# Kernel optimization log

Measured on AMD Instinct MI355X. Metric: run time of the kernel, lower is better.

## Reference

```python
import jax, jax.numpy as jnp
import numpy as np

NB = 8          # num_bins
HID = 128       # hidden channels of coupling ResidualNet
TB = 3.0        # tail_bound
MINB = 1e-3     # min bin width / height
MIND = 1e-3     # min derivative
DCONST = float(np.log(np.exp(1.0 - MIND) - 1.0))  # softplus(DCONST)+MIND == 1
LU_EPS = 1e-3


def rqs_inverse(x, uw, uh, ud):
    """Inverse monotonic rational-quadratic spline with linear tails (nflows math).
    x: [B,F]; uw,uh broadcastable to [B,F,NB]; ud broadcastable to [B,F,NB-1]."""
    K = NB
    uw = jnp.broadcast_to(uw, x.shape + (K,))
    uh = jnp.broadcast_to(uh, x.shape + (K,))
    ud = jnp.broadcast_to(ud, x.shape + (K - 1,))
    ud = jnp.pad(ud, [(0, 0)] * x.ndim + [(1, 1)], constant_values=DCONST)  # boundary derivs = 1
    inside = (x >= -TB) & (x <= TB)
    xi = jnp.clip(x, -TB, TB)

    def knots(u):
        v = MINB + (1.0 - MINB * K) * jax.nn.softmax(u, -1)
        c = jnp.concatenate([jnp.zeros(x.shape + (1,), x.dtype), jnp.cumsum(v, -1)], -1)
        c = 2.0 * TB * c - TB
        c = c.at[..., 0].set(-TB).at[..., -1].set(TB)
        return c, c[..., 1:] - c[..., :-1]

    cw, w = knots(uw)   # x-knots / bin widths
    ch, h = knots(uh)   # y-knots / bin heights
    d = MIND + jax.nn.softplus(ud)  # [B,F,K+1] knot derivatives

    # searchsorted on cumheights (inverse direction)
    locs = ch.at[..., -1].add(1e-6)
    idx = jnp.clip(jnp.sum((xi[..., None] >= locs).astype(jnp.int32), -1) - 1, 0, K - 1)[..., None]
    g = lambda a: jnp.take_along_axis(a, idx, -1)[..., 0]
    in_cw, in_w, in_ch, in_h = g(cw), g(w), g(ch), g(h)
    delta = in_h / in_w
    d0 = g(d)
    d1 = jnp.take_along_axis(d, idx + 1, -1)[..., 0]

    t = xi - in_ch
    s = d0 + d1 - 2.0 * delta
    a = t * s + in_h * (delta - d0)
    b = in_h * d0 - t * s
    c = -delta * t
    root = (2.0 * c) / (-b - jnp.sqrt(b * b - 4.0 * a * c))
    out = root * in_w + in_cw
    tm = root * (1.0 - root)
    den = delta + s * tm
    dnum = delta ** 2 * (d1 * root ** 2 + 2.0 * delta * tm + d0 * (1.0 - root) ** 2)
    ld = -(jnp.log(dnum) - 2.0 * jnp.log(den))
    return jnp.where(inside, out, x), jnp.where(inside, ld, 0.0)


def resnet(x, Wi, bi, Wb, bb, Wo, bo):
    # nflows ResidualNet: initial linear, 2 pre-activation residual blocks, final linear
    t = x @ Wi + bi
    for j in range(2):
        r = jax.nn.relu(t) @ Wb[2 * j] + bb[2 * j]
        r = jax.nn.relu(r) @ Wb[2 * j + 1] + bb[2 * j + 1]
        t = t + r
    return t @ Wo + bo


def coupling_inverse(z, Wi, bi, Wb, bb, Wo, bo, uw_u, uh_u, ud_u):
    # alternating mask: even dims = identity split, odd dims = transform split
    ident, trans = z[:, 0::2], z[:, 1::2]
    # unconditional spline on identity features is inverted FIRST, then feeds the net
    ident, ld_u = rqs_inverse(ident, uw_u, uh_u, ud_u)
    B, F = trans.shape
    p = resnet(ident, Wi, bi, Wb, bb, Wo, bo).reshape(B, F, 3 * NB - 1)
    scale = 1.0 / np.sqrt(HID)  # nflows divides widths/heights by sqrt(hidden_features)
    trans, ld_t = rqs_inverse(trans, p[..., :NB] * scale, p[..., NB:2 * NB] * scale, p[..., 2 * NB:])
    out = jnp.stack([ident, trans], -1).reshape(B, -1)
    return out, jnp.sum(ld_u, -1) + jnp.sum(ld_t, -1)


def log_prob(x, loc, log_scale, Wi, bi, Wb, bb, Wo, bo, uw_u, uh_u, ud_u,
             lu_lower, lu_upper, lu_ud, lu_b, perms):
    N, T, D = x.shape
    z = x.reshape(-1, D)
    lq = jnp.zeros((z.shape[0],), x.dtype)
    for i in (2, 1, 0):  # flows = [C0,LU0,C1,LU1,C2,LU2]; invert in reverse order
        # LULinearPermute.inverse: permute, then y = L(Ux) + b, logdet = sum log diag(U)
        zp = z[:, perms[i]]
        diag = jax.nn.softplus(lu_ud[i]) + LU_EPS
        U = jnp.triu(lu_upper[i], 1) + jnp.diag(diag)
        L = jnp.tril(lu_lower[i], -1) + jnp.eye(D, dtype=x.dtype)
        z = (zp @ U.T) @ L.T + lu_b[i]
        lq = lq + jnp.sum(jnp.log(diag))
        z, ld = coupling_inverse(z, Wi[i], bi[i], Wb[i], bb[i], Wo[i], bo[i],
                                 uw_u[i], uh_u[i], ud_u[i])
        lq = lq + ld
    # DiagGaussian base log-prob
    lq = lq - 0.5 * D * jnp.log(2.0 * jnp.pi) \
            - jnp.sum(log_scale + 0.5 * ((z - loc) / jnp.exp(log_scale)) ** 2, -1)
    return lq.reshape(N, T)


def setup_inputs():
    key = jax.random.key(0)
    ks = jax.random.split(key, 16)
    N, T, D, F = 8, 512, 550, 275
    OUT = F * (3 * NB - 1)
    s = 0.1
    return {
        "x": jax.random.normal(ks[0], (N, T, D), jnp.float32),
        "loc": 0.1 * jax.random.normal(ks[1], (D,), jnp.float32),
        "log_scale": jnp.zeros((D,), jnp.float32),
        "Wi": s * jax.random.normal(ks[2], (3, F, HID), jnp.float32),
        "bi": jnp.zeros((3, HID), jnp.float32),
        "Wb": s * jax.random.normal(ks[3], (3, 4, HID, HID), jnp.float32),
        "bb": jnp.zeros((3, 4, HID), jnp.float32),
        "Wo": 0.01 * jax.random.normal(ks[4], (3, HID, OUT), jnp.float32),
        "bo": 0.01 * jax.random.normal(ks[5], (3, OUT), jnp.float32),
        "uw_u": jax.random.uniform(ks[6], (3, F, NB), jnp.float32),
        "uh_u": jax.random.uniform(ks[7], (3, F, NB), jnp.float32),
        "ud_u": jax.random.uniform(ks[8], (3, F, NB - 1), jnp.float32),
        "lu_lower": 0.05 * jax.random.normal(ks[9], (3, D, D), jnp.float32),
        "lu_upper": 0.05 * jax.random.normal(ks[10], (3, D, D), jnp.float32),
        "lu_ud": jnp.full((3, D), DCONST, jnp.float32),
        "lu_b": jnp.zeros((3, D), jnp.float32),
        "perms": jnp.stack([jax.random.permutation(ks[11 + i], D) for i in range(3)]).astype(jnp.int32),
    }


def reference(x, loc, log_scale, Wi, bi, Wb, bb, Wo, bo, uw_u, uh_u, ud_u,
              lu_lower, lu_upper, lu_ud, lu_b, perms):
    # log_prob(x).reshape(N, T); calculate_likelihood would just apply exp/nan->0/clamp on top.
    return log_prob(x, loc, log_scale, Wi, bi, Wb, bb, Wo, bo, uw_u, uh_u, ud_u,
                    lu_lower, lu_upper, lu_ud, lu_b, perms)
```

## Files before the change

### kernel.cpp

```cpp
#include <hip/hip_runtime.h>


#define D_DIM 550
#define D_PAD 576
#define N_PAD_A 640
#define F_DIM 275
#define F_PAD 320
#define FP_HALF 288
#define HID_DIM 128
#define OUT_DIM 6325
#define OUT_PAD 6400
#define FT_PAD 276
#define WO2_ROWS (FT_PAD*32)
#define WO_GX (WO2_ROWS/128)
#define B_ROWS 4096
#define NBINS 8
#define TB_C 3.0f
#define MINB_C 0.001f
#define MIND_C 0.001f
#define DCONST_C 0.53974233f
#define LUEPS_C 0.001f
#define RSQRT_HID 0.08838834764831845f

typedef unsigned short ushort_t;
typedef __attribute__((ext_vector_type(8))) short short8;
typedef __attribute__((ext_vector_type(8))) unsigned short ushort8;
typedef __attribute__((ext_vector_type(4))) unsigned short ushort4v;
typedef __attribute__((ext_vector_type(4))) float f32x4;

__device__ __forceinline__ ushort_t f2bf(float f){
    union{float f; unsigned u;} v; v.f = f;
    unsigned r = v.u + 0x7fffu + ((v.u>>16)&1u);
    return (ushort_t)(r>>16);
}
__device__ __forceinline__ float bf2f(ushort_t h){
    union{unsigned u; float f;} v; v.u = ((unsigned)h)<<16;
    return v.f;
}
__device__ __forceinline__ float softplusf(float x){
    return fmaxf(x, 0.f) + __logf(1.f + __expf(-fabsf(x)));
}

__device__ __forceinline__ void knots_from_u(const float* u, float* c, float* w){
    float m = u[0];
#pragma unroll
    for(int k=1;k<NBINS;k++) m = fmaxf(m, u[k]);
    float e[NBINS]; float s = 0.f;
#pragma unroll
    for(int k=0;k<NBINS;k++){ e[k] = __expf(u[k]-m); s += e[k]; }
    float inv = 1.f/s;
    float cum = 0.f;
    c[0] = -TB_C;
#pragma unroll
    for(int k=0;k<NBINS;k++){
        float v = MINB_C + (1.f - MINB_C*(float)NBINS)*e[k]*inv;
        cum += v;
        c[k+1] = 2.f*TB_C*cum - TB_C;
    }
    c[NBINS] = TB_C;
#pragma unroll
    for(int k=0;k<NBINS;k++) w[k] = c[k+1]-c[k];
}

__device__ __forceinline__ void rqs_inv(float x,
                                        const float* cw, const float* w,
                                        const float* ch, const float* h,
                                        const float* d,
                                        float& out, float& ld){
    bool inside = (x >= -TB_C) && (x <= TB_C);
    float xi = fminf(fmaxf(x, -TB_C), TB_C);
    int idx = 0;
#pragma unroll
    for(int j=1;j<NBINS;j++) idx += (xi >= ch[j]) ? 1 : 0;
    float icw=cw[0], iw=w[0], ich=ch[0], ih=h[0], d0=d[0], d1=d[1];
#pragma unroll
    for(int j=1;j<NBINS;j++){
        if(idx==j){ icw=cw[j]; iw=w[j]; ich=ch[j]; ih=h[j]; d0=d[j]; d1=d[j+1]; }
    }
    float delta = ih/iw;
    float t  = xi - ich;
    float s  = d0 + d1 - 2.f*delta;
    float a  = t*s + ih*(delta - d0);
    float b  = ih*d0 - t*s;
    float c  = -delta*t;
    float disc = b*b - 4.f*a*c;
    float root = 2.f*c / (-b - sqrtf(fmaxf(disc, 0.f)));
    float o  = root*iw + icw;
    float tm = root*(1.f-root);
    float den  = delta + s*tm;
    float dnum = delta*delta*(d1*root*root + 2.f*delta*tm + d0*(1.f-root)*(1.f-root));
    float l = 2.f*__logf(den) - __logf(dnum);
    out = inside ? o : x;
    ld  = inside ? l : 0.f;
}


__global__ void build_knots_kernel(const float* __restrict__ uw_u,
                                   const float* __restrict__ uh_u,
                                   const float* __restrict__ ud_u,
                                   float* __restrict__ knots){
    int g = blockIdx.x*blockDim.x + threadIdx.x;
    if(g >= 3*F_DIM) return;
    float* kb = knots + (size_t)g*43;
    float c[9], w[8];
    knots_from_u(uw_u + (size_t)g*8, c, w);
#pragma unroll
    for(int k=0;k<9;k++) kb[k]=c[k];
#pragma unroll
    for(int k=0;k<8;k++) kb[9+k]=w[k];
    knots_from_u(uh_u + (size_t)g*8, c, w);
#pragma unroll
    for(int k=0;k<9;k++) kb[17+k]=c[k];
#pragma unroll
    for(int k=0;k<8;k++) kb[26+k]=w[k];
    float dend = MIND_C + softplusf(DCONST_C);
    kb[34]=dend; kb[42]=dend;
    const float* ud = ud_u + (size_t)g*7;
#pragma unroll
    for(int k=0;k<7;k++) kb[35+k] = MIND_C + softplusf(ud[k]);
}

__global__ void logdiag_kernel(const float* __restrict__ lu_ud, float* __restrict__ outv){
    int tid = threadIdx.x;
    float s = 0.f;
    for(int k=tid; k<3*D_DIM; k+=256) s += __logf(softplusf(lu_ud[k]) + LUEPS_C);
#pragma unroll
    for(int o=32;o>0;o>>=1) s += __shfl_down(s, o);
    __shared__ float sm[4];
    if((tid&63)==0) sm[tid>>6]=s;
    __syncthreads();
    if(tid==0) outv[0] = sm[0]+sm[1]+sm[2]+sm[3];
}

__global__ void build_LU_bf16(const float* __restrict__ lower,
                              const float* __restrict__ upper,
                              const float* __restrict__ ud,
                              const int* __restrict__ perm,
                              ushort_t* __restrict__ Lmb,
                              ushort_t* __restrict__ UpTb){
    int l = blockIdx.z;
    lower += (size_t)l*D_DIM*D_DIM; upper += (size_t)l*D_DIM*D_DIM;
    ud += (size_t)l*D_DIM; perm += (size_t)l*D_DIM;
    Lmb += (size_t)l*N_PAD_A*D_PAD; UpTb += (size_t)l*N_PAD_A*D_PAD;
    int k = blockIdx.x*blockDim.x + threadIdx.x;
    int j = blockIdx.y;
    if(k >= D_DIM) return;
    float lv = (j>k) ? lower[(size_t)j*D_DIM+k] : (j==k ? 1.f : 0.f);
    Lmb[(size_t)j*D_PAD+k] = f2bf(lv);
    float uv;
    if(j<k)       uv = upper[(size_t)j*D_DIM+k];
    else if(j==k) uv = softplusf(ud[k]) + LUEPS_C;
    else          uv = 0.f;
    UpTb[(size_t)perm[k]*D_PAD + j] = f2bf(uv);
}

__global__ void convert_pad(const float* __restrict__ in, ushort_t* __restrict__ out,
                            int M, int K, int Mpad, int Kpad){
    int idx = blockIdx.x*256 + threadIdx.x;
    if(idx >= Mpad*Kpad) return;
    int r = idx / Kpad, c = idx - r*Kpad;
    float v = (r<M && c<K) ? in[(size_t)r*K+c] : 0.f;
    out[idx] = f2bf(v);
}

template<int REMAP>
__global__ void transpose_convert(const float* __restrict__ in, ushort_t* __restrict__ out,
                                  int K, int N, int Kpad, int Npad, long s_in, long s_out){
    in += (size_t)blockIdx.z*s_in; out += (size_t)blockIdx.z*s_out;
    __shared__ float t[32][33];
    int kb = blockIdx.x*32, nb = blockIdx.y*32;
    int tx = threadIdx.x, ty = threadIdx.y;
#pragma unroll
    for(int i=0;i<32;i+=8){
        int k = kb+ty+i, n = nb+tx;
        t[ty+i][tx] = (k<K && n<N) ? in[(size_t)k*N+n] : 0.f;
    }
    __syncthreads();
#pragma unroll
    for(int i=0;i<32;i+=8){
        int n = nb+ty+i, k = kb+tx;
        if(REMAP){
            if(n < OUT_DIM && k < Kpad){
                int f = n/23, j = n - 23*f;
                out[(size_t)(f*32+j)*Kpad+k] = f2bf(t[tx][ty+i]);
            }
        } else if(n<Npad && k<Kpad){
            out[(size_t)n*Kpad+k] = f2bf(t[tx][ty+i]);
        }
    }
}

__global__ void reorder_bias(const float* __restrict__ bo, float* __restrict__ bo2){
    int idx = blockIdx.x*256 + threadIdx.x;
    if(idx >= 3*OUT_DIM) return;
    int l = idx/OUT_DIM, n = idx%OUT_DIM;
    int f = n/23, j = n - 23*f;
    bo2[(size_t)l*WO2_ROWS + f*32 + j] = bo[idx];
}

template<int OUTBF>
__global__ __launch_bounds__(256)
void gemm_mfma(const ushort_t* __restrict__ A, const ushort_t* __restrict__ Bt,
               const float* __restrict__ bias, void* __restrict__ Cv,
               int M, int N, int Kpad, long sA, long sB, long sC){
    A  += (size_t)blockIdx.z*sA;
    Bt += (size_t)blockIdx.z*sB;
    __shared__ ushort_t As[128][72];
    __shared__ ushort_t Bs[128][72];
    int tid = threadIdx.x;
    int row0 = blockIdx.y*128, col0 = blockIdx.x*128;
    int wave = tid>>6, lane = tid&63;
    int wm = wave&1, wn = wave>>1;
    int lm = lane&15, quad = lane>>4;
    f32x4 acc[4][4] = {};
    for(int k0=0; k0<Kpad; k0+=64){
#pragma unroll
        for(int it=0; it<4; it++){
            int c = tid + it*256;
            int r = c>>3, c8 = (c&7)*8;
            *(ushort8*)&As[r][c8] = *(const ushort8*)(A + (size_t)(row0+r)*Kpad + k0 + c8);
            *(ushort8*)&Bs[r][c8] = *(const ushort8*)(Bt + (size_t)(col0+r)*Kpad + k0 + c8);
        }
        __syncthreads();
#pragma unroll
        for(int ks=0; ks<2; ks++){
            short8 af[4], bfr[4];
#pragma unroll
            for(int i=0;i<4;i++){
                af[i]  = *(const short8*)&As[wm*64 + i*16 + lm][ks*32 + quad*8];
                bfr[i] = *(const short8*)&Bs[wn*64 + i*16 + lm][ks*32 + quad*8];
            }
#pragma unroll
            for(int i=0;i<4;i++)
#pragma unroll
                for(int j=0;j<4;j++)
                    acc[i][j] = __builtin_amdgcn_mfma_f32_16x16x32_bf16(af[i], bfr[j], acc[i][j], 0, 0, 0);
        }
        __syncthreads();
    }
#pragma unroll
    for(int i=0;i<4;i++){
        int rbase = row0 + wm*64 + i*16 + quad*4;
#pragma unroll
        for(int j=0;j<4;j++){
            int gc = col0 + wn*64 + j*16 + lm;
            if(gc >= N) continue;
            float bv = bias[gc];
#pragma unroll
            for(int r=0;r<4;r++){
                int gr = rbase + r;
                float v = acc[i][j][r] + bv;
                if(OUTBF) ((ushort_t*)Cv + (size_t)blockIdx.z*sC)[(size_t)gr*N+gc] = f2bf(v);
                else      ((float*)Cv + (size_t)blockIdx.z*sC)[(size_t)gr*N+gc] = v;
            }
        }
    }
}

__global__ __launch_bounds__(256)
void resnet_fused(const ushort_t* __restrict__ identb,
                  const ushort_t* __restrict__ WiT,
                  const float* __restrict__ bi,
                  const ushort_t* __restrict__ WbT,
                  const float* __restrict__ bb,
                  ushort_t* __restrict__ tb){
    __shared__ __align__(16) char smem[(64*136 + 128*136)*2];
    ushort_t (*As2)[136] = (ushort_t(*)[136])smem;
    ushort_t (*Ws)[136]  = (ushort_t(*)[136])(smem + 64*136*2);
    ushort_t (*As1)[72]  = (ushort_t(*)[72])smem;
    ushort_t (*Bs1)[72]  = (ushort_t(*)[72])(smem + 64*136*2);
    int tid = threadIdx.x, wave = tid>>6, lane = tid&63;
    int lm = lane&15, quad = lane>>4;
    int r0 = blockIdx.x*64;
    f32x4 cur[8] = {};
    f32x4 tsv[8];
    for(int k0=0; k0<F_PAD; k0+=64){
#pragma unroll
        for(int it=0; it<2; it++){
            int v = tid + it*256; int r = v>>3, c8 = (v&7)*8;
            *(ushort8*)&As1[r][c8] = *(const ushort8*)(identb + (size_t)(r0+r)*F_PAD + k0 + c8);
        }
#pragma unroll
        for(int it=0; it<4; it++){
            int v = tid + it*256; int n = v>>3, c8 = (v&7)*8;
            *(ushort8*)&Bs1[n][c8] = *(const ushort8*)(WiT + (size_t)n*F_PAD + k0 + c8);
        }
        __syncthreads();
#pragma unroll
        for(int ks=0; ks<2; ks++){
            short8 af = *(const short8*)&As1[wave*16 + lm][ks*32 + quad*8];
#pragma unroll
            for(int j=0;j<8;j++){
                short8 bf = *(const short8*)&Bs1[j*16 + lm][ks*32 + quad*8];
                cur[j] = __builtin_amdgcn_mfma_f32_16x16x32_bf16(af, bf, cur[j], 0, 0, 0);
            }
        }
        __syncthreads();
    }
#pragma unroll
    for(int j=0;j<8;j++){
        float bv = bi[j*16 + lm];
#pragma unroll
        for(int r=0;r<4;r++) cur[j][r] += bv;
        tsv[j] = cur[j];
    }
    for(int st=0; st<4; st++){
#pragma unroll
        for(int j=0;j<8;j++)
#pragma unroll
            for(int r=0;r<4;r++)
                As2[wave*16 + quad*4 + r][j*16 + lm] = f2bf(fmaxf(cur[j][r], 0.f));
#pragma unroll
        for(int it=0; it<8; it++){
            int v = tid + it*256; int n = v>>4, c8 = (v&15)*8;
            *(ushort8*)&Ws[n][c8] = *(const ushort8*)(WbT + (size_t)st*128*128 + (size_t)n*128 + c8);
        }
        __syncthreads();
        f32x4 acc[8] = {};
#pragma unroll
        for(int ks=0; ks<4; ks++){
            short8 af = *(const short8*)&As2[wave*16 + lm][ks*32 + quad*8];
#pragma unroll
            for(int j=0;j<8;j++){
                short8 bf = *(const short8*)&Ws[j*16 + lm][ks*32 + quad*8];
                acc[j] = __builtin_amdgcn_mfma_f32_16x16x32_bf16(af, bf, acc[j], 0, 0, 0);
            }
        }
        __syncthreads();
#pragma unroll
        for(int j=0;j<8;j++){
            float bv = bb[st*128 + j*16 + lm];
#pragma unroll
            for(int r=0;r<4;r++) acc[j][r] += bv;
        }
        if(st==1 || st==3){
#pragma unroll
            for(int j=0;j<8;j++){
#pragma unroll
                for(int r=0;r<4;r++) acc[j][r] += tsv[j][r];
                tsv[j] = acc[j];
            }
        }
#pragma unroll
        for(int j=0;j<8;j++) cur[j] = acc[j];
    }
#pragma unroll
    for(int j=0;j<8;j++)
#pragma unroll
        for(int r=0;r<4;r++)
            tb[(size_t)(r0 + wave*16 + quad*4 + r)*HID_DIM + j*16 + lm] = f2bf(cur[j][r]);
}

__global__ __launch_bounds__(256)
void zodd_transpose(const float* __restrict__ z2, float* __restrict__ z2oddT){
    __shared__ float s[32][65];
    int r0 = blockIdx.x*64, f0 = blockIdx.y*32;
    int tid = threadIdx.x;
    int f = tid & 31, rb = tid >> 5;
#pragma unroll
    for(int rr=0; rr<8; rr++){
        int r = rb + rr*8;
        int fg = f0 + f;
        float v = (fg < F_DIM) ? z2[(size_t)(r0+r)*D_DIM + 2*fg + 1] : 0.f;
        s[f][r] = v;
    }
    __syncthreads();
    int lane = tid & 63, fb = tid >> 6;
#pragma unroll
    for(int ff=0; ff<8; ff++){
        int fo = fb + ff*4;
        z2oddT[(size_t)(f0+fo)*B_ROWS + r0 + lane] = s[fo][lane];
    }
}

__global__ __launch_bounds__(256, 2)
void wo_spline(const ushort_t* __restrict__ tb,
               const ushort_t* __restrict__ Wo2,
               const float* __restrict__ bo2,
               const float* __restrict__ z2oddT,
               ushort_t* __restrict__ zOddT,
               float* __restrict__ ldpart){
    __shared__ __align__(16) char smem[128*133*4];
    __shared__ float ldred[128];
    ushort_t (*As)[72] = (ushort_t(*)[72])smem;
    ushort_t (*Bs)[72] = (ushort_t(*)[72])(smem + 128*72*2);
    float (*P)[133] = (float(*)[133])smem;
    int tid = threadIdx.x;
    int flat = blockIdx.y*WO_GX + blockIdx.x;
    int flat2 = (flat & 7)*(WO_GX*32/8) + (flat >> 3);
    int cbl = flat2 % WO_GX;
    int rbl = flat2 / WO_GX;
    int row0 = rbl*128, col0 = cbl*128;
    int wave = tid>>6, lane = tid&63;
    int wm = wave&1, wn = wave>>1;
    int lm = lane&15, quad = lane>>4;
    f32x4 acc[4][4] = {};
    for(int k0=0; k0<HID_DIM; k0+=64){
#pragma unroll
        for(int it=0; it<4; it++){
            int c = tid + it*256;
            int r = c>>3, c8 = (c&7)*8;
            *(ushort8*)&As[r][c8] = *(const ushort8*)(tb + (size_t)(row0+r)*HID_DIM + k0 + c8);
            *(ushort8*)&Bs[r][c8] = *(const ushort8*)(Wo2 + (size_t)(col0+r)*HID_DIM + k0 + c8);
        }
        __syncthreads();
#pragma unroll
        for(int ks=0; ks<2; ks++){
            short8 af[4], bfr[4];
#pragma unroll
            for(int i=0;i<4;i++){
                af[i]  = *(const short8*)&As[wm*64 + i*16 + lm][ks*32 + quad*8];
                bfr[i] = *(const short8*)&Bs[wn*64 + i*16 + lm][ks*32 + quad*8];
            }
#pragma unroll
            for(int i=0;i<4;i++)
#pragma unroll
                for(int j=0;j<4;j++)
                    acc[i][j] = __builtin_amdgcn_mfma_f32_16x16x32_bf16(af[i], bfr[j], acc[i][j], 0, 0, 0);
        }
        __syncthreads();
    }
#pragma unroll
    for(int j=0;j<4;j++){
        int cl = wn*64 + j*16 + lm;
        float bv = bo2[col0 + cl];
#pragma unroll
        for(int i=0;i<4;i++){
            int rl = wm*64 + i*16 + quad*4;
#pragma unroll
            for(int r=0;r<4;r++) P[rl+r][cl] = acc[i][j][r] + bv;
        }
    }
    __syncthreads();
    int row = tid & 127;
    int fbase = col0 >> 5;
    float ldsum = 0.f;
    const float dend = MIND_C + softplusf(DCONST_C);
#pragma unroll
    for(int e2=0;e2<2;e2++){
        int feat = (tid>>7) + e2*2;
        int fg = fbase + feat;
        if(fg < F_DIM){
            const float* q = &P[row][feat*32];
            float xv = z2oddT[(size_t)fg*B_ROWS + row0 + row];
            bool inside = (xv >= -TB_C) && (xv <= TB_C);
            float xi = fminf(fmaxf(xv, -TB_C), TB_C);
            float eh[8];
            float mh = -1e30f, sh = 0.f;
#pragma unroll
            for(int k=0;k<8;k++){ float u = q[8+k]*RSQRT_HID; eh[k]=u; mh=fmaxf(mh,u); }
#pragma unroll
            for(int k=0;k<8;k++){ eh[k] = __expf(eh[k]-mh); sh += eh[k]; }
            float invh = (1.f - MINB_C*8.f)/sh;
            int idx = 0;
            {
                float cum = 0.f;
#pragma unroll
                for(int k=0;k<7;k++){
                    cum += MINB_C + eh[k]*invh;
                    float ck = 2.f*TB_C*cum - TB_C;
                    idx += (xi >= ck) ? 1 : 0;
                }
            }
            float ich = -TB_C, ihh = 0.f;
            {
                float cum = 0.f, cprev = -TB_C;
#pragma unroll
                for(int k=0;k<8;k++){
                    cum += MINB_C + eh[k]*invh;
                    float ck = (k==7) ? TB_C : (2.f*TB_C*cum - TB_C);
                    if(idx==k){ ich = cprev; ihh = ck - cprev; }
                    cprev = ck;
                }
            }
            float ew[8];
            float mw = -1e30f, sw = 0.f;
#pragma unroll
            for(int k=0;k<8;k++){ float u = q[k]*RSQRT_HID; ew[k]=u; mw=fmaxf(mw,u); }
#pragma unroll
            for(int k=0;k<8;k++){ ew[k] = __expf(ew[k]-mw); sw += ew[k]; }
            float invw = (1.f - MINB_C*8.f)/sw;
            float icw = -TB_C, iww = 0.f;
            {
                float cum = 0.f, cprev = -TB_C;
#pragma unroll
                for(int k=0;k<8;k++){
                    cum += MINB_C + ew[k]*invw;
                    float ck = (k==7) ? TB_C : (2.f*TB_C*cum - TB_C);
                    if(idx==k){ icw = cprev; iww = ck - cprev; }
                    cprev = ck;
                }
            }
            float d0 = (idx==0) ? dend : (MIND_C + softplusf(q[15+idx]));
            float d1 = (idx==7) ? dend : (MIND_C + softplusf(q[16+idx]));
            float delta = ihh/iww;
            float t  = xi - ich;
            float s  = d0 + d1 - 2.f*delta;
            float a  = t*s + ihh*(delta - d0);
            float b  = ihh*d0 - t*s;
            float c  = -delta*t;
            float disc = fmaxf(b*b - 4.f*a*c, 0.f);
            float root = 2.f*c / (-b - sqrtf(disc));
            float o  = root*iww + icw;
            float tm = root*(1.f-root);
            float den  = delta + s*tm;
            float dnum = delta*delta*(d1*root*root + 2.f*delta*tm + d0*(1.f-root)*(1.f-root));
            float l = 2.f*__logf(den) - __logf(dnum);
            zOddT[(size_t)fg*B_ROWS + row0 + row] = f2bf(inside ? o : xv);
            ldsum += inside ? l : 0.f;
        }
    }
    if(tid >= 128) ldred[tid-128] = ldsum;
    __syncthreads();
    if(tid < 128) ldpart[(size_t)cbl*B_ROWS + row0 + tid] = ldsum + ldred[tid];
}

__global__ __launch_bounds__(256)
void interleave_z(const ushort_t* __restrict__ identb,
                  const ushort_t* __restrict__ zOddT,
                  const float* __restrict__ ldpart,
                  ushort_t* __restrict__ znb,
                  float* __restrict__ lq){
    __shared__ ushort_t s[FP_HALF][34];
    int r0 = blockIdx.x*32;
    int tid = threadIdx.x;
#pragma unroll
    for(int i=0;i<36;i++){
        int idx = tid + i*256;
        int f = idx>>5, r = idx&31;
        s[f][r] = zOddT[(size_t)f*B_ROWS + r0 + r];
    }
    __syncthreads();
    int wv = tid>>6, lane = tid&63;
#pragma unroll
    for(int k=0;k<8;k++){
        int r = wv + k*4;
        const ushort_t* idr = identb + (size_t)(r0+r)*F_PAD;
        unsigned* orow = (unsigned*)(znb + (size_t)(r0+r)*D_PAD);
#pragma unroll
        for(int c=0;c<5;c++){
            int f = lane + c*64;
            if(f < FP_HALF){
                unsigned lo = idr[f];
                unsigned hi = s[f][r];
                orow[f] = lo | (hi<<16);
            }
        }
    }
    if(tid < 32){
        float acc = 0.f;
        for(int cb=0; cb<WO_GX; cb++)
            acc += ldpart[(size_t)cb*B_ROWS + r0 + tid];
        lq[r0 + tid] += acc;
    }
}


__global__ __launch_bounds__(320)
void ident_spline_kernel(const float* __restrict__ z2, const float* __restrict__ knots,
                         int layer, ushort_t* __restrict__ identb,
                         float* __restrict__ lq){
    int row = blockIdx.x; int tid = threadIdx.x;
    float ldv = 0.f;
    if(tid < F_DIM){
        const float* kb = knots + ((size_t)(layer*F_DIM + tid))*43;
        float x = z2[(size_t)row*D_DIM + 2*tid];
        float o, l;
        rqs_inv(x, kb, kb+9, kb+17, kb+26, kb+34, o, l);
        identb[(size_t)row*F_PAD + tid] = f2bf(o);
        ldv = l;
    } else {
        identb[(size_t)row*F_PAD + tid] = 0;
    }
    __shared__ float sm[5];
    float v = ldv;
#pragma unroll
    for(int o=32;o>0;o>>=1) v += __shfl_down(v, o);
    if((tid&63)==0) sm[tid>>6]=v;
    __syncthreads();
    if(tid==0) lq[row] += sm[0]+sm[1]+sm[2]+sm[3]+sm[4];
}

__global__ __launch_bounds__(320)
void finalize_kernel(const ushort_t* __restrict__ zb, const float* __restrict__ loc,
                     const float* __restrict__ lsc, const float* __restrict__ lq,
                     const float* __restrict__ logdiag, float* __restrict__ out){
    int row = blockIdx.x; int tid = threadIdx.x;
    float s = 0.f;
    for(int k=tid; k<D_DIM; k+=320){
        float l = lsc[k];
        float diff = (bf2f(zb[(size_t)row*D_PAD+k])-loc[k])*__expf(-l);
        s += l + 0.5f*diff*diff;
    }
    __shared__ float sm[5];
#pragma unroll
    for(int o=32;o>0;o>>=1) s += __shfl_down(s, o);
    if((tid&63)==0) sm[tid>>6]=s;
    __syncthreads();
    if(tid==0){
        float tot = sm[0]+sm[1]+sm[2]+sm[3]+sm[4];
        out[row] = lq[row] + logdiag[0] - 275.f*1.8378770664f - tot;
    }
}


extern "C" void kernel_launch(void* const* d_in, const int* in_sizes, int n_in,
                              void* d_out, int out_size, void* d_ws, size_t ws_size,
                              hipStream_t stream){
    const float* x        = (const float*)d_in[0];
    const float* loc      = (const float*)d_in[1];
    const float* lsc      = (const float*)d_in[2];
    const float* Wi       = (const float*)d_in[3];
    const float* bi       = (const float*)d_in[4];
    const float* Wb       = (const float*)d_in[5];
    const float* bb       = (const float*)d_in[6];
    const float* Wo       = (const float*)d_in[7];
    const float* bo       = (const float*)d_in[8];
    const float* uw_u     = (const float*)d_in[9];
    const float* uh_u     = (const float*)d_in[10];
    const float* ud_u     = (const float*)d_in[11];
    const float* lu_lower = (const float*)d_in[12];
    const float* lu_upper = (const float*)d_in[13];
    const float* lu_ud    = (const float*)d_in[14];
    const float* lu_b     = (const float*)d_in[15];
    const int*   perms    = (const int*)d_in[16];
    float* out = (float*)d_out;

    char* base = (char*)d_ws;
    size_t off = 0;
    auto alloc = [&](size_t bytes)->char*{
        char* p = base + off;
        off += (bytes + 255) & ~(size_t)255;
        return p;
    };
    float* lq      = (float*)alloc(B_ROWS*4);
    float* zbias   = (float*)alloc(D_PAD*4);
    float* logdiag = (float*)alloc(64*4);
    float* knots   = (float*)alloc((size_t)3*F_DIM*43*4);
    float* z2      = (float*)alloc((size_t)B_ROWS*D_DIM*4);
    float* z2oddT  = (float*)alloc((size_t)FP_HALF*B_ROWS*4);
    float* ldpart  = (float*)alloc((size_t)WO_GX*B_ROWS*4);
    float* bo2     = (float*)alloc((size_t)3*WO2_ROWS*4);
    ushort_t* xb   = (ushort_t*)alloc((size_t)B_ROWS*D_PAD*2);
    ushort_t* zbf0 = (ushort_t*)alloc((size_t)B_ROWS*D_PAD*2);
    ushort_t* zbf1 = (ushort_t*)alloc((size_t)B_ROWS*D_PAD*2);
    ushort_t* zOddT= (ushort_t*)alloc((size_t)FP_HALF*B_ROWS*2);
    ushort_t* Lmb  = (ushort_t*)alloc((size_t)3*N_PAD_A*D_PAD*2);
    ushort_t* UpTb = (ushort_t*)alloc((size_t)3*N_PAD_A*D_PAD*2);
    ushort_t* Apb  = (ushort_t*)alloc((size_t)3*N_PAD_A*D_PAD*2);
    ushort_t* identb=(ushort_t*)alloc((size_t)B_ROWS*F_PAD*2);
    ushort_t* tb   = (ushort_t*)alloc((size_t)B_ROWS*HID_DIM*2);
    ushort_t* WiT  = (ushort_t*)alloc((size_t)3*HID_DIM*F_PAD*2);
    ushort_t* WbT  = (ushort_t*)alloc((size_t)3*4*HID_DIM*HID_DIM*2);
    ushort_t* Wo2  = (ushort_t*)alloc((size_t)3*WO2_ROWS*HID_DIM*2);

    hipMemsetAsync(lq, 0, B_ROWS*sizeof(float), stream);
    hipMemsetAsync(zbias, 0, D_PAD*sizeof(float), stream);
    hipMemsetAsync(zOddT, 0, (size_t)FP_HALF*B_ROWS*2, stream);
    hipMemsetAsync(Lmb, 0, (size_t)3*N_PAD_A*D_PAD*2, stream);
    hipMemsetAsync(UpTb, 0, (size_t)3*N_PAD_A*D_PAD*2, stream);
    hipMemsetAsync(Wo2, 0, (size_t)3*WO2_ROWS*HID_DIM*2, stream);
    hipMemsetAsync(bo2, 0, (size_t)3*WO2_ROWS*4, stream);
    build_knots_kernel<<<dim3((3*F_DIM+255)/256), dim3(256), 0, stream>>>(uw_u, uh_u, ud_u, knots);
    logdiag_kernel<<<dim3(1), dim3(256), 0, stream>>>(lu_ud, logdiag);
    convert_pad<<<dim3((B_ROWS*D_PAD+255)/256), dim3(256), 0, stream>>>(
        x, xb, B_ROWS, D_DIM, B_ROWS, D_PAD);
    build_LU_bf16<<<dim3((D_DIM+255)/256, D_DIM, 3), dim3(256), 0, stream>>>(
        lu_lower, lu_upper, lu_ud, perms, Lmb, UpTb);
    gemm_mfma<1><<<dim3(5, 5, 3), dim3(256), 0, stream>>>(
        Lmb, UpTb, zbias, Apb, N_PAD_A, D_PAD, D_PAD,
        (long)N_PAD_A*D_PAD, (long)N_PAD_A*D_PAD, (long)N_PAD_A*D_PAD);
    dim3 tthr(32,8);
    transpose_convert<0><<<dim3(F_PAD/32, HID_DIM/32, 3), tthr, 0, stream>>>(
        Wi, WiT, F_DIM, HID_DIM, F_PAD, HID_DIM, (long)F_DIM*HID_DIM, (long)F_PAD*HID_DIM);
    transpose_convert<0><<<dim3(HID_DIM/32, HID_DIM/32, 12), tthr, 0, stream>>>(
        Wb, WbT, HID_DIM, HID_DIM, HID_DIM, HID_DIM, (long)HID_DIM*HID_DIM, (long)HID_DIM*HID_DIM);
    transpose_convert<1><<<dim3(HID_DIM/32, OUT_PAD/32, 3), tthr, 0, stream>>>(
        Wo, Wo2, HID_DIM, OUT_DIM, HID_DIM, OUT_PAD, (long)HID_DIM*OUT_DIM, (long)WO2_ROWS*HID_DIM);
    reorder_bias<<<dim3((3*OUT_DIM+255)/256), dim3(256), 0, stream>>>(bo, bo2);

    const ushort_t* zcur_b = xb;
    ushort_t* zbf[2] = {zbf0, zbf1};
    int zi = 0;

    for(int it=0; it<3; ++it){
        int i = 2 - it;

        gemm_mfma<0><<<dim3(N_PAD_A/128, B_ROWS/128), dim3(256), 0, stream>>>(
            zcur_b, Apb + (size_t)i*N_PAD_A*D_PAD, lu_b + (size_t)i*D_DIM,
            z2, B_ROWS, D_DIM, D_PAD, 0, 0, 0);

        zodd_transpose<<<dim3(B_ROWS/64, FP_HALF/32), dim3(256), 0, stream>>>(
            z2, z2oddT);

        ident_spline_kernel<<<dim3(B_ROWS), dim3(320), 0, stream>>>(
            z2, knots, i, identb, lq);

        resnet_fused<<<dim3(B_ROWS/64), dim3(256), 0, stream>>>(
            identb, WiT + (size_t)i*HID_DIM*F_PAD, bi + (size_t)i*HID_DIM,
            WbT + (size_t)i*4*HID_DIM*HID_DIM, bb + (size_t)i*4*HID_DIM, tb);

        wo_spline<<<dim3(WO_GX, B_ROWS/128), dim3(256), 0, stream>>>(
            tb, Wo2 + (size_t)i*WO2_ROWS*HID_DIM, bo2 + (size_t)i*WO2_ROWS,
            z2oddT, zOddT, ldpart);

        interleave_z<<<dim3(B_ROWS/32), dim3(256), 0, stream>>>(
            identb, zOddT, ldpart, zbf[zi], lq);

        zcur_b = zbf[zi];
        zi ^= 1;
    }

    finalize_kernel<<<dim3(B_ROWS), dim3(320), 0, stream>>>(
        zcur_b, loc, lsc, lq, logdiag, out);
}
```

Baseline: 434.5 us.

## Shrink resnet row tile to 16, keep weights in registers, tile-transpose UT build

The fused ResNet kernel now handles 16 rows per block instead of 64, launching four times as many blocks. Each wave owns two output column tiles and loads its weight fragments straight from global memory into registers, double-buffering the next stage's weights, so shared memory holds only the 16-row activation tile. Separately, building the permuted transposed U matrix is split into its own kernel that transposes through a shared-memory tile, which avoids the scattered strided writes of the old combined kernel. The aim is more parallelism and less shared-memory traffic, at the cost of each block re-reading the weights from global memory or L2.

```diff
diff --git a/kernel.cpp b/kernel.cpp
--- a/kernel.cpp
+++ b/kernel.cpp
@@ -132,26 +132,45 @@
     if(tid==0) outv[0] = sm[0]+sm[1]+sm[2]+sm[3];
 }
 
-__global__ void build_LU_bf16(const float* __restrict__ lower,
-                              const float* __restrict__ upper,
-                              const float* __restrict__ ud,
-                              const int* __restrict__ perm,
-                              ushort_t* __restrict__ Lmb,
-                              ushort_t* __restrict__ UpTb){
+__global__ void build_L_bf16(const float* __restrict__ lower,
+                             ushort_t* __restrict__ Lmb){
     int l = blockIdx.z;
-    lower += (size_t)l*D_DIM*D_DIM; upper += (size_t)l*D_DIM*D_DIM;
-    ud += (size_t)l*D_DIM; perm += (size_t)l*D_DIM;
-    Lmb += (size_t)l*N_PAD_A*D_PAD; UpTb += (size_t)l*N_PAD_A*D_PAD;
+    lower += (size_t)l*D_DIM*D_DIM;
+    Lmb += (size_t)l*N_PAD_A*D_PAD;
     int k = blockIdx.x*blockDim.x + threadIdx.x;
     int j = blockIdx.y;
     if(k >= D_DIM) return;
     float lv = (j>k) ? lower[(size_t)j*D_DIM+k] : (j==k ? 1.f : 0.f);
     Lmb[(size_t)j*D_PAD+k] = f2bf(lv);
-    float uv;
-    if(j<k)       uv = upper[(size_t)j*D_DIM+k];
-    else if(j==k) uv = softplusf(ud[k]) + LUEPS_C;
-    else          uv = 0.f;
-    UpTb[(size_t)perm[k]*D_PAD + j] = f2bf(uv);
+}
+
+__global__ void build_UT_bf16(const float* __restrict__ upper,
+                              const float* __restrict__ ud,
+                              const int* __restrict__ perm,
+                              ushort_t* __restrict__ UpTb){
+    int l = blockIdx.z;
+    upper += (size_t)l*D_DIM*D_DIM; ud += (size_t)l*D_DIM; perm += (size_t)l*D_DIM;
+    UpTb += (size_t)l*N_PAD_A*D_PAD;
+    __shared__ float t[32][33];
+    int j0 = blockIdx.x*32, k0 = blockIdx.y*32;
+    int tx = threadIdx.x, ty = threadIdx.y;
+#pragma unroll
+    for(int i=0;i<32;i+=8){
+        int j = j0+ty+i, k = k0+tx;
+        float uv = 0.f;
+        if(j<D_DIM && k<D_DIM){
+            if(j<k)       uv = upper[(size_t)j*D_DIM+k];
+            else if(j==k) uv = softplusf(ud[k]) + LUEPS_C;
+        }
+        t[ty+i][tx] = uv;
+    }
+    __syncthreads();
+#pragma unroll
+    for(int i=0;i<32;i+=8){
+        int k = k0+ty+i, j = j0+tx;
+        if(k<D_DIM)
+            UpTb[(size_t)perm[k]*D_PAD + j] = f2bf(t[tx][ty+i]);
+    }
 }
 
 __global__ void convert_pad(const float* __restrict__ in, ushort_t* __restrict__ out,
@@ -264,91 +283,97 @@
                   const ushort_t* __restrict__ WbT,
                   const float* __restrict__ bb,
                   ushort_t* __restrict__ tb){
-    __shared__ __align__(16) char smem[(64*136 + 128*136)*2];
-    ushort_t (*As2)[136] = (ushort_t(*)[136])smem;
-    ushort_t (*Ws)[136]  = (ushort_t(*)[136])(smem + 64*136*2);
-    ushort_t (*As1)[72]  = (ushort_t(*)[72])smem;
-    ushort_t (*Bs1)[72]  = (ushort_t(*)[72])(smem + 64*136*2);
+    __shared__ ushort_t As2[16][136];
     int tid = threadIdx.x, wave = tid>>6, lane = tid&63;
     int lm = lane&15, quad = lane>>4;
-    int r0 = blockIdx.x*64;
-    f32x4 cur[8] = {};
-    f32x4 tsv[8];
+    int r0 = blockIdx.x*16;
+    int arow = r0 + lm;
+    f32x4 cur[2] = {};
+    f32x4 tsv[2];
     for(int k0=0; k0<F_PAD; k0+=64){
-#pragma unroll
-        for(int it=0; it<2; it++){
-            int v = tid + it*256; int r = v>>3, c8 = (v&7)*8;
-            *(ushort8*)&As1[r][c8] = *(const ushort8*)(identb + (size_t)(r0+r)*F_PAD + k0 + c8);
-        }
-#pragma unroll
-        for(int it=0; it<4; it++){
-            int v = tid + it*256; int n = v>>3, c8 = (v&7)*8;
-            *(ushort8*)&Bs1[n][c8] = *(const ushort8*)(WiT + (size_t)n*F_PAD + k0 + c8);
-        }
+        const ushort_t* ap = identb + (size_t)arow*F_PAD + k0 + quad*8;
+        short8 af0 = *(const short8*)(ap);
+        short8 af1 = *(const short8*)(ap + 32);
+#pragma unroll
+        for(int jj=0;jj<2;jj++){
+            int n = (wave*2+jj)*16 + lm;
+            const ushort_t* wp = WiT + (size_t)n*F_PAD + k0 + quad*8;
+            short8 b0 = *(const short8*)(wp);
+            short8 b1 = *(const short8*)(wp + 32);
+            cur[jj] = __builtin_amdgcn_mfma_f32_16x16x32_bf16(af0, b0, cur[jj], 0, 0, 0);
+            cur[jj] = __builtin_amdgcn_mfma_f32_16x16x32_bf16(af1, b1, cur[jj], 0, 0, 0);
+        }
+    }
+#pragma unroll
+    for(int jj=0;jj<2;jj++){
+        float bv = bi[(wave*2+jj)*16 + lm];
+#pragma unroll
+        for(int r=0;r<4;r++) cur[jj][r] += bv;
+        tsv[jj] = cur[jj];
+    }
+    short8 wA[2][4], wB[2][4];
+#pragma unroll
+    for(int jj=0;jj<2;jj++){
+        int n = (wave*2+jj)*16 + lm;
+        const ushort_t* wp = WbT + (size_t)n*128 + quad*8;
+#pragma unroll
+        for(int ks=0;ks<4;ks++) wA[jj][ks] = *(const short8*)(wp + ks*32);
+    }
+#pragma unroll
+    for(int st=0; st<4; st++){
         __syncthreads();
 #pragma unroll
-        for(int ks=0; ks<2; ks++){
-            short8 af = *(const short8*)&As1[wave*16 + lm][ks*32 + quad*8];
-#pragma unroll
-            for(int j=0;j<8;j++){
-                short8 bf = *(const short8*)&Bs1[j*16 + lm][ks*32 + quad*8];
-                cur[j] = __builtin_amdgcn_mfma_f32_16x16x32_bf16(af, bf, cur[j], 0, 0, 0);
+        for(int jj=0;jj<2;jj++)
+#pragma unroll
+            for(int r=0;r<4;r++)
+                As2[quad*4 + r][(wave*2+jj)*16 + lm] = f2bf(fmaxf(cur[jj][r], 0.f));
+        if(st < 3){
+#pragma unroll
+            for(int jj=0;jj<2;jj++){
+                int n = (wave*2+jj)*16 + lm;
+                const ushort_t* wp = WbT + (size_t)(st+1)*128*128 + (size_t)n*128 + quad*8;
+#pragma unroll
+                for(int ks=0;ks<4;ks++){
+                    if(st & 1) wA[jj][ks] = *(const short8*)(wp + ks*32);
+                    else       wB[jj][ks] = *(const short8*)(wp + ks*32);
+                }
             }
         }
         __syncthreads();
-    }
-#pragma unroll
-    for(int j=0;j<8;j++){
-        float bv = bi[j*16 + lm];
-#pragma unroll
-        for(int r=0;r<4;r++) cur[j][r] += bv;
-        tsv[j] = cur[j];
-    }
-    for(int st=0; st<4; st++){
-#pragma unroll
-        for(int j=0;j<8;j++)
-#pragma unroll
-            for(int r=0;r<4;r++)
-                As2[wave*16 + quad*4 + r][j*16 + lm] = f2bf(fmaxf(cur[j][r], 0.f));
-#pragma unroll
-        for(int it=0; it<8; it++){
-            int v = tid + it*256; int n = v>>4, c8 = (v&15)*8;
-            *(ushort8*)&Ws[n][c8] = *(const ushort8*)(WbT + (size_t)st*128*128 + (size_t)n*128 + c8);
-        }
-        __syncthreads();
-        f32x4 acc[8] = {};
-#pragma unroll
-        for(int ks=0; ks<4; ks++){
-            short8 af = *(const short8*)&As2[wave*16 + lm][ks*32 + quad*8];
-#pragma unroll
-            for(int j=0;j<8;j++){
-                short8 bf = *(const short8*)&Ws[j*16 + lm][ks*32 + quad*8];
-                acc[j] = __builtin_amdgcn_mfma_f32_16x16x32_bf16(af, bf, acc[j], 0, 0, 0);
-            }
-        }
-        __syncthreads();
-#pragma unroll
-        for(int j=0;j<8;j++){
-            float bv = bb[st*128 + j*16 + lm];
-#pragma unroll
-            for(int r=0;r<4;r++) acc[j][r] += bv;
+        short8 af[4];
+#pragma unroll
+        for(int ks=0;ks<4;ks++) af[ks] = *(const short8*)&As2[lm][ks*32 + quad*8];
+        f32x4 acc[2] = {};
+#pragma unroll
+        for(int ks=0;ks<4;ks++){
+#pragma unroll
+            for(int jj=0;jj<2;jj++){
+                short8 bf = (st & 1) ? wB[jj][ks] : wA[jj][ks];
+                acc[jj] = __builtin_amdgcn_mfma_f32_16x16x32_bf16(af[ks], bf, acc[jj], 0, 0, 0);
+            }
+        }
+#pragma unroll
+        for(int jj=0;jj<2;jj++){
+            float bv = bb[st*128 + (wave*2+jj)*16 + lm];
+#pragma unroll
+            for(int r=0;r<4;r++) acc[jj][r] += bv;
         }
         if(st==1 || st==3){
 #pragma unroll
-            for(int j=0;j<8;j++){
-#pragma unroll
-                for(int r=0;r<4;r++) acc[j][r] += tsv[j][r];
-                tsv[j] = acc[j];
-            }
-        }
-#pragma unroll
-        for(int j=0;j<8;j++) cur[j] = acc[j];
-    }
-#pragma unroll
-    for(int j=0;j<8;j++)
+            for(int jj=0;jj<2;jj++){
+#pragma unroll
+                for(int r=0;r<4;r++) acc[jj][r] += tsv[jj][r];
+                tsv[jj] = acc[jj];
+            }
+        }
+#pragma unroll
+        for(int jj=0;jj<2;jj++) cur[jj] = acc[jj];
+    }
+#pragma unroll
+    for(int jj=0;jj<2;jj++)
 #pragma unroll
         for(int r=0;r<4;r++)
-            tb[(size_t)(r0 + wave*16 + quad*4 + r)*HID_DIM + j*16 + lm] = f2bf(cur[j][r]);
+            tb[(size_t)(r0 + quad*4 + r)*HID_DIM + (wave*2+jj)*16 + lm] = f2bf(cur[jj][r]);
 }
 
 __global__ __launch_bounds__(256)
@@ -665,12 +690,14 @@
     logdiag_kernel<<<dim3(1), dim3(256), 0, stream>>>(lu_ud, logdiag);
     convert_pad<<<dim3((B_ROWS*D_PAD+255)/256), dim3(256), 0, stream>>>(
         x, xb, B_ROWS, D_DIM, B_ROWS, D_PAD);
-    build_LU_bf16<<<dim3((D_DIM+255)/256, D_DIM, 3), dim3(256), 0, stream>>>(
-        lu_lower, lu_upper, lu_ud, perms, Lmb, UpTb);
+    build_L_bf16<<<dim3((D_DIM+255)/256, D_DIM, 3), dim3(256), 0, stream>>>(
+        lu_lower, Lmb);
+    dim3 tthr(32,8);
+    build_UT_bf16<<<dim3(18, 18, 3), tthr, 0, stream>>>(
+        lu_upper, lu_ud, perms, UpTb);
     gemm_mfma<1><<<dim3(5, 5, 3), dim3(256), 0, stream>>>(
         Lmb, UpTb, zbias, Apb, N_PAD_A, D_PAD, D_PAD,
         (long)N_PAD_A*D_PAD, (long)N_PAD_A*D_PAD, (long)N_PAD_A*D_PAD);
-    dim3 tthr(32,8);
     transpose_convert<0><<<dim3(F_PAD/32, HID_DIM/32, 3), tthr, 0, stream>>>(
         Wi, WiT, F_DIM, HID_DIM, F_PAD, HID_DIM, (long)F_DIM*HID_DIM, (long)F_PAD*HID_DIM);
     transpose_convert<0><<<dim3(HID_DIM/32, HID_DIM/32, 12), tthr, 0, stream>>>(
@@ -696,7 +723,7 @@
         ident_spline_kernel<<<dim3(B_ROWS), dim3(320), 0, stream>>>(
             z2, knots, i, identb, lq);
 
-        resnet_fused<<<dim3(B_ROWS/64), dim3(256), 0, stream>>>(
+        resnet_fused<<<dim3(B_ROWS/16), dim3(256), 0, stream>>>(
             identb, WiT + (size_t)i*HID_DIM*F_PAD, bi + (size_t)i*HID_DIM,
             WbT + (size_t)i*4*HID_DIM*HID_DIM, bb + (size_t)i*4*HID_DIM, tb);
 
```

After: 428.7 us. Within noise of the previous version (-1.3%).
